# Optimization experiments

Measured on AMD Instinct MI355X. Metric: run time of the kernel, lower is better.

## Reference

```python
import jax, jax.numpy as jnp
import numpy as np

B, T, V, E, H = 32, 40, 8000, 50, 2048


def setup_inputs() -> dict:
    key = jax.random.key(0)
    ks = jax.random.split(key, 13)
    s = 0.02  # small init scale for stability
    return {
        "features": jax.random.normal(ks[0], (B, H), dtype=jnp.float32),
        "captions": jax.random.randint(ks[1], (B, T), 0, V),
        "emb": jax.random.normal(ks[2], (V, E), dtype=jnp.float32) * s,
        "lstm_Wih": jax.random.normal(ks[3], (4 * H, E), dtype=jnp.float32) * s,
        "lstm_bih": jax.random.normal(ks[4], (4 * H,), dtype=jnp.float32) * s,
        "lstm_Whh": jax.random.normal(ks[5], (4 * H, H), dtype=jnp.float32) * s,
        "lstm_bhh": jax.random.normal(ks[6], (4 * H,), dtype=jnp.float32) * s,
        "gru_Wih": jax.random.normal(ks[7], (3 * H, H), dtype=jnp.float32) * s,
        "gru_bih": jax.random.normal(ks[8], (3 * H,), dtype=jnp.float32) * s,
        "gru_Whh": jax.random.normal(ks[9], (3 * H, H), dtype=jnp.float32) * s,
        "gru_bhh": jax.random.normal(ks[10], (3 * H,), dtype=jnp.float32) * s,
        "lin_W": jax.random.normal(ks[11], (V, H), dtype=jnp.float32) * s,
        "lin_b": jax.random.normal(ks[12], (V,), dtype=jnp.float32) * s,
    }


def reference(features, captions, emb, lstm_Wih, lstm_bih, lstm_Whh, lstm_bhh,
              gru_Wih, gru_bih, gru_Whh, gru_bhh, lin_W, lin_b):
    # Dropout layers act as identity in eval mode.
    embeddings = emb[captions]                 # [B, T, E]
    xs = jnp.swapaxes(embeddings[:, :-1], 0, 1)  # [T-1, B, E]

    def step(carry, x):
        h_l, c_l, h_g = carry
        # torch LSTMCell
        gates = x @ lstm_Wih.T + lstm_bih + h_l @ lstm_Whh.T + lstm_bhh
        i, f, g, o = jnp.split(gates, 4, axis=-1)
        c = jax.nn.sigmoid(f) * c_l + jax.nn.sigmoid(i) * jnp.tanh(g)
        h = jax.nn.sigmoid(o) * jnp.tanh(c)
        # torch GRUCell, input = lstm cell state c
        gi = c @ gru_Wih.T + gru_bih
        gh = h_g @ gru_Whh.T + gru_bhh
        r_i, z_i, n_i = jnp.split(gi, 3, axis=-1)
        r_h, z_h, n_h = jnp.split(gh, 3, axis=-1)
        r = jax.nn.sigmoid(r_i + r_h)
        z = jax.nn.sigmoid(z_i + z_h)
        n = jnp.tanh(n_i + r * n_h)
        hg = (1.0 - z) * n + z * h_g
        out = hg @ lin_W.T + lin_b              # [B, V]
        return (h, c, hg), out

    init = (features, features, features)
    _, outs = jax.lax.scan(step, init, xs)      # [T-1, B, V]
    return jnp.swapaxes(outs, 0, 1)             # [B, T-1, V]
```

## Files before the change

### kernel.cpp

```cpp
#include <hip/hip_runtime.h>

#define BB 32
#define TT 40
#define TS 39
#define VV 8000
#define EE 50
#define HH 2048

typedef short s16x8 __attribute__((ext_vector_type(8)));
typedef float f32x4 __attribute__((ext_vector_type(4)));

__device__ __forceinline__ float sigmf(float x) { return 1.0f / (1.0f + __expf(-x)); }
__device__ __forceinline__ float tanhf_fast(float x) { return 2.0f / (1.0f + __expf(-2.0f * x)) - 1.0f; }

__device__ __forceinline__ unsigned short f2bf(float x) {
    union { float f; unsigned u; } v; v.f = x;
    unsigned r = v.u + 0x7FFF + ((v.u >> 16) & 1);
    return (unsigned short)(r >> 16);
}

__global__ void convert_kernel(const float* __restrict__ src,
                               unsigned short* __restrict__ dst, int n4) {
    int i = blockIdx.x * 256 + threadIdx.x;
    if (i < n4) {
        float4 v = ((const float4*)src)[i];
        ushort4 o;
        o.x = f2bf(v.x); o.y = f2bf(v.y); o.z = f2bf(v.z); o.w = f2bf(v.w);
        ((ushort4*)dst)[i] = o;
    }
}

__global__ void embed_proj_kernel(const int* __restrict__ caps,
                                  const float* __restrict__ emb,
                                  const float* __restrict__ Wih,
                                  const float* __restrict__ bih,
                                  const float* __restrict__ bhh,
                                  float* __restrict__ xw) {
    __shared__ float elds[BB][EE];
    int t = blockIdx.y;
    int j = blockIdx.x * 256 + threadIdx.x;
    for (int idx = threadIdx.x; idx < BB * EE; idx += 256) {
        int bl = idx / EE, e = idx - bl * EE;
        elds[bl][e] = emb[(size_t)caps[bl * TT + t] * EE + e];
    }
    __syncthreads();
    float wreg[EE];
#pragma unroll
    for (int e = 0; e < EE; ++e) wreg[e] = Wih[(size_t)j * EE + e];
    float bias = bih[j] + bhh[j];
    for (int bl = 0; bl < BB; ++bl) {
        float acc = bias;
#pragma unroll
        for (int e = 0; e < EE; ++e) acc += wreg[e] * elds[bl][e];
        xw[((size_t)(t * BB + bl)) * (4 * HH) + j] = acc;
    }
}

__global__ void init_state_kernel(const float* __restrict__ feat,
                                  float* __restrict__ c32, float* __restrict__ hg32,
                                  unsigned short* __restrict__ hbf,
                                  unsigned short* __restrict__ cbf,
                                  unsigned short* __restrict__ hgbf) {
    int i = blockIdx.x * 256 + threadIdx.x;
    float v = feat[i];
    c32[i] = v; hg32[i] = v;
    unsigned short b = f2bf(v);
    hbf[i] = b; cbf[i] = b; hgbf[i] = b;
}

__global__ __launch_bounds__(1024, 4) void step1_kernel(
    const unsigned short* __restrict__ Whh,
    const unsigned short* __restrict__ gWhh,
    const float* __restrict__ gbhh,
    const float* __restrict__ xw_t,
    const unsigned short* __restrict__ hbf_in,
    const unsigned short* __restrict__ hgbf,
    float* __restrict__ c32,
    unsigned short* __restrict__ cbf,
    unsigned short* __restrict__ hbf_out,
    float* __restrict__ gh)
{
    __shared__ float lsum[4][4][32][17];
    const int tid = threadIdx.x;
    const int lane = tid & 63;
    const int w = tid >> 6;
    const int g = w >> 2;
    const int kh = w & 3;
    const int l15 = lane & 15;
    const int lq = lane >> 4;
    const int kofs = kh * 512 + lq * 8;

    const bool lstm = (blockIdx.x < 128);
    const unsigned short* Abase;
    const unsigned short* Brow;
    if (lstm) {
        int kk0 = blockIdx.x * 16;
        Brow = Whh + (size_t)(g * HH + kk0 + l15) * HH + kofs;
        Abase = hbf_in;
    } else {
        int n0 = (blockIdx.x - 128) * 64;
        Brow = gWhh + (size_t)(n0 + g * 16 + l15) * HH + kofs;
        Abase = hgbf;
    }
    const unsigned short* Arow0 = Abase + l15 * HH + kofs;
    const unsigned short* Arow1 = Arow0 + 16 * HH;

    f32x4 acc0 = {0.f, 0.f, 0.f, 0.f};
    f32x4 acc1 = {0.f, 0.f, 0.f, 0.f};
#pragma unroll 4
    for (int it = 0; it < 16; ++it) {
        s16x8 bv = *(const s16x8*)(Brow + it * 32);
        s16x8 a0 = *(const s16x8*)(Arow0 + it * 32);
        s16x8 a1 = *(const s16x8*)(Arow1 + it * 32);
        acc0 = __builtin_amdgcn_mfma_f32_16x16x32_bf16(a0, bv, acc0, 0, 0, 0);
        acc1 = __builtin_amdgcn_mfma_f32_16x16x32_bf16(a1, bv, acc1, 0, 0, 0);
    }
#pragma unroll
    for (int r = 0; r < 4; ++r) {
        lsum[g][kh][lq * 4 + r][l15]      = acc0[r];
        lsum[g][kh][16 + lq * 4 + r][l15] = acc1[r];
    }
    __syncthreads();

    if (lstm) {
        if (tid < 512) {
            int kk0 = blockIdx.x * 16;
            int kkl = tid & 15, b = tid >> 4;
            int kk = kk0 + kkl;
            const float* xwb = xw_t + (size_t)b * 4 * HH;
            float vi = lsum[0][0][b][kkl] + lsum[0][1][b][kkl] + lsum[0][2][b][kkl] + lsum[0][3][b][kkl] + xwb[kk];
            float vf = lsum[1][0][b][kkl] + lsum[1][1][b][kkl] + lsum[1][2][b][kkl] + lsum[1][3][b][kkl] + xwb[HH + kk];
            float vg = lsum[2][0][b][kkl] + lsum[2][1][b][kkl] + lsum[2][2][b][kkl] + lsum[2][3][b][kkl] + xwb[2 * HH + kk];
            float vo = lsum[3][0][b][kkl] + lsum[3][1][b][kkl] + lsum[3][2][b][kkl] + lsum[3][3][b][kkl] + xwb[3 * HH + kk];
            int idx = b * HH + kk;
            float c = sigmf(vf) * c32[idx] + sigmf(vi) * tanhf_fast(vg);
            float h = sigmf(vo) * tanhf_fast(c);
            c32[idx] = c;
            cbf[idx] = f2bf(c);
            hbf_out[idx] = f2bf(h);
        }
    } else {
        int n0 = (blockIdx.x - 128) * 64;
        for (int cell = tid; cell < 2048; cell += 1024) {
            int nl = cell & 63, b = cell >> 6;
            int s = nl >> 4, n15 = nl & 15;
            float v = lsum[s][0][b][n15] + lsum[s][1][b][n15] + lsum[s][2][b][n15] + lsum[s][3][b][n15]
                      + gbhh[n0 + nl];
            gh[b * 3 * HH + n0 + nl] = v;
        }
    }
}

__global__ __launch_bounds__(768, 3) void step2_kernel(
    const unsigned short* __restrict__ gWih,
    const float* __restrict__ gbih,
    const unsigned short* __restrict__ cbf,
    const float* __restrict__ gh,
    float* __restrict__ hg32,
    unsigned short* __restrict__ hgbf,
    unsigned short* __restrict__ hg_all_t)
{
    __shared__ float lsum[3][4][32][17];
    const int tid = threadIdx.x;
    const int lane = tid & 63;
    const int w = tid >> 6;
    const int g = w >> 2;
    const int kh = w & 3;
    const int l15 = lane & 15;
    const int lq = lane >> 4;
    const int kofs = kh * 512 + lq * 8;
    const int kk0 = blockIdx.x * 16;

    const unsigned short* Arow0 = cbf + l15 * HH + kofs;
    const unsigned short* Arow1 = Arow0 + 16 * HH;
    const unsigned short* Brow = gWih + (size_t)(g * HH + kk0 + l15) * HH + kofs;

    f32x4 acc0 = {0.f, 0.f, 0.f, 0.f};
    f32x4 acc1 = {0.f, 0.f, 0.f, 0.f};
#pragma unroll 4
    for (int it = 0; it < 16; ++it) {
        s16x8 bv = *(const s16x8*)(Brow + it * 32);
        s16x8 a0 = *(const s16x8*)(Arow0 + it * 32);
        s16x8 a1 = *(const s16x8*)(Arow1 + it * 32);
        acc0 = __builtin_amdgcn_mfma_f32_16x16x32_bf16(a0, bv, acc0, 0, 0, 0);
        acc1 = __builtin_amdgcn_mfma_f32_16x16x32_bf16(a1, bv, acc1, 0, 0, 0);
    }
#pragma unroll
    for (int r = 0; r < 4; ++r) {
        lsum[g][kh][lq * 4 + r][l15]      = acc0[r];
        lsum[g][kh][16 + lq * 4 + r][l15] = acc1[r];
    }
    __syncthreads();

    if (tid < 512) {
        int kkl = tid & 15, b = tid >> 4;
        int kk = kk0 + kkl;
        float ri = lsum[0][0][b][kkl] + lsum[0][1][b][kkl] + lsum[0][2][b][kkl] + lsum[0][3][b][kkl] + gbih[kk];
        float zi = lsum[1][0][b][kkl] + lsum[1][1][b][kkl] + lsum[1][2][b][kkl] + lsum[1][3][b][kkl] + gbih[HH + kk];
        float ni = lsum[2][0][b][kkl] + lsum[2][1][b][kkl] + lsum[2][2][b][kkl] + lsum[2][3][b][kkl] + gbih[2 * HH + kk];
        const float* ghb = gh + b * 3 * HH;
        float r = sigmf(ri + ghb[kk]);
        float z = sigmf(zi + ghb[HH + kk]);
        float n = tanhf_fast(ni + r * ghb[2 * HH + kk]);
        int idx = b * HH + kk;
        float hgn = (1.f - z) * n + z * hg32[idx];
        hg32[idx] = hgn;
        unsigned short hb = f2bf(hgn);
        hgbf[idx] = hb;
        hg_all_t[idx] = hb;
    }
}

__global__ __launch_bounds__(256) void out_gemm_kernel(
    const unsigned short* __restrict__ A,
    const unsigned short* __restrict__ Wl,
    const float* __restrict__ bl,
    float* __restrict__ out) {
    __shared__ unsigned short As[128][32];
    __shared__ unsigned short Bs[128][32];
    const int tid = threadIdx.x;
    const int lane = tid & 63;
    const int w = tid >> 6;
    const int l15 = lane & 15;
    const int lq = lane >> 4;
    const int mt = blockIdx.x, nt = blockIdx.y;
    const int mq = w >> 1, nq = w & 1;

    const int row0 = tid >> 2, kc0 = (tid & 3) * 8;
    const unsigned short* Ap0 = A + (size_t)(mt * 128 + row0) * HH + kc0;
    const unsigned short* Ap1 = A + (size_t)(mt * 128 + 64 + row0) * HH + kc0;
    const unsigned short* Bp0 = Wl + (size_t)(nt * 128 + row0) * HH + kc0;
    const unsigned short* Bp1 = Wl + (size_t)(nt * 128 + 64 + row0) * HH + kc0;

    f32x4 acc[4][4];
#pragma unroll
    for (int i = 0; i < 4; ++i)
#pragma unroll
        for (int j = 0; j < 4; ++j) acc[i][j] = (f32x4){0.f, 0.f, 0.f, 0.f};

    for (int k0 = 0; k0 < HH; k0 += 32) {
        s16x8 a0v = *(const s16x8*)(Ap0 + k0);
        s16x8 a1v = *(const s16x8*)(Ap1 + k0);
        s16x8 b0v = *(const s16x8*)(Bp0 + k0);
        s16x8 b1v = *(const s16x8*)(Bp1 + k0);
        *(s16x8*)&As[row0][kc0]      = a0v;
        *(s16x8*)&As[64 + row0][kc0] = a1v;
        *(s16x8*)&Bs[row0][kc0]      = b0v;
        *(s16x8*)&Bs[64 + row0][kc0] = b1v;
        __syncthreads();
        s16x8 af[4], bf[4];
#pragma unroll
        for (int i = 0; i < 4; ++i) af[i] = *(const s16x8*)&As[mq * 64 + i * 16 + l15][lq * 8];
#pragma unroll
        for (int j = 0; j < 4; ++j) bf[j] = *(const s16x8*)&Bs[nq * 64 + j * 16 + l15][lq * 8];
#pragma unroll
        for (int i = 0; i < 4; ++i)
#pragma unroll
            for (int j = 0; j < 4; ++j)
                acc[i][j] = __builtin_amdgcn_mfma_f32_16x16x32_bf16(af[i], bf[j], acc[i][j], 0, 0, 0);
        __syncthreads();
    }
#pragma unroll
    for (int j = 0; j < 4; ++j) {
        int n = nt * 128 + nq * 64 + j * 16 + l15;
        float bn = bl[n < VV ? n : VV - 1];
#pragma unroll
        for (int i = 0; i < 4; ++i) {
#pragma unroll
            for (int r = 0; r < 4; ++r) {
                int m = mt * 128 + mq * 64 + i * 16 + lq * 4 + r;
                if (m < TS * BB && n < VV) {
                    int t = m >> 5, b = m & 31;
                    out[((size_t)b * TS + t) * VV + n] = acc[i][j][r] + bn;
                }
            }
        }
    }
}

extern "C" void kernel_launch(void* const* d_in, const int* in_sizes, int n_in,
                              void* d_out, int out_size, void* d_ws, size_t ws_size,
                              hipStream_t stream) {
    const float* features = (const float*)d_in[0];
    const int*   captions = (const int*)d_in[1];
    const float* emb      = (const float*)d_in[2];
    const float* lstm_Wih = (const float*)d_in[3];
    const float* lstm_bih = (const float*)d_in[4];
    const float* lstm_Whh = (const float*)d_in[5];
    const float* lstm_bhh = (const float*)d_in[6];
    const float* gru_Wih  = (const float*)d_in[7];
    const float* gru_bih  = (const float*)d_in[8];
    const float* gru_Whh  = (const float*)d_in[9];
    const float* gru_bhh  = (const float*)d_in[10];
    const float* lin_W    = (const float*)d_in[11];
    const float* lin_b    = (const float*)d_in[12];
    float* out = (float*)d_out;

    unsigned short* us = (unsigned short*)d_ws;
    unsigned short* Whh_bf  = us;
    unsigned short* gWhh_bf = Whh_bf  + (size_t)8192 * HH;
    unsigned short* gWih_bf = gWhh_bf + (size_t)6144 * HH;
    unsigned short* linW_bf = gWih_bf + (size_t)6144 * HH;
    unsigned short* hbf0    = linW_bf + (size_t)VV * HH;
    unsigned short* hbf1    = hbf0 + BB * HH;
    unsigned short* cbf     = hbf1 + BB * HH;
    unsigned short* hgbf    = cbf  + BB * HH;
    unsigned short* hg_all  = hgbf + BB * HH;
    float* f32s = (float*)(hg_all + (size_t)1280 * HH);
    float* xw   = f32s;
    float* c32  = xw + (size_t)TS * BB * 4 * HH;
    float* hg32 = c32 + BB * HH;
    float* gh   = hg32 + BB * HH;

    {
        int n4;
        n4 = 8192 * HH / 4;
        convert_kernel<<<(n4 + 255) / 256, 256, 0, stream>>>(lstm_Whh, Whh_bf, n4);
        n4 = 6144 * HH / 4;
        convert_kernel<<<(n4 + 255) / 256, 256, 0, stream>>>(gru_Whh, gWhh_bf, n4);
        convert_kernel<<<(n4 + 255) / 256, 256, 0, stream>>>(gru_Wih, gWih_bf, n4);
        n4 = VV * HH / 4;
        convert_kernel<<<(n4 + 255) / 256, 256, 0, stream>>>(lin_W, linW_bf, n4);
    }

    embed_proj_kernel<<<dim3(4 * HH / 256, TS), 256, 0, stream>>>(
        captions, emb, lstm_Wih, lstm_bih, lstm_bhh, xw);

    init_state_kernel<<<(BB * HH) / 256, 256, 0, stream>>>(
        features, c32, hg32, hbf0, cbf, hgbf);

    for (int t = 0; t < TS; ++t) {
        const unsigned short* hin = (t & 1) ? hbf1 : hbf0;
        unsigned short*       hout = (t & 1) ? hbf0 : hbf1;
        step1_kernel<<<224, 1024, 0, stream>>>(
            Whh_bf, gWhh_bf, gru_bhh, xw + (size_t)t * BB * 4 * HH,
            hin, hgbf, c32, cbf, hout, gh);
        step2_kernel<<<128, 768, 0, stream>>>(
            gWih_bf, gru_bih, cbf, gh, hg32, hgbf, hg_all + (size_t)t * BB * HH);
    }

    out_gemm_kernel<<<dim3((TS * BB + 127) / 128, (VV + 127) / 128), 256, 0, stream>>>(
        hg_all, linW_bf, lin_b, out);
}
```

Baseline: 2.053 ms.

## Fuse per-timestep recurrence kernels into one persistent kernel with grid barriers

Replaces the 78 per-step launches of step1/step2 with one persistent recurrence kernel of 224 blocks that loops over all timesteps. An atomic-counter grid barrier separates the LSTM/GRU-hidden phase from the GRU-input phase. This removes kernel launch overhead and inter-kernel gaps. In exchange, all blocks must be co-resident or the barrier deadlocks, and the spin barrier adds its own latency. Non-LSTM blocks sit idle during the second phase.

Result: slower. 3.850 ms (+87.6%).

```diff
diff --git a/kernel.cpp b/kernel.cpp
--- a/kernel.cpp
+++ b/kernel.cpp
@@ -6,6 +6,7 @@
 #define VV 8000
 #define EE 50
 #define HH 2048
+#define NBLK 224
 
 typedef short s16x8 __attribute__((ext_vector_type(8)));
 typedef float f32x4 __attribute__((ext_vector_type(4)));
@@ -60,25 +61,42 @@
                                   float* __restrict__ c32, float* __restrict__ hg32,
                                   unsigned short* __restrict__ hbf,
                                   unsigned short* __restrict__ cbf,
-                                  unsigned short* __restrict__ hgbf) {
+                                  unsigned short* __restrict__ hgbf,
+                                  unsigned int* __restrict__ bar) {
     int i = blockIdx.x * 256 + threadIdx.x;
     float v = feat[i];
     c32[i] = v; hg32[i] = v;
     unsigned short b = f2bf(v);
     hbf[i] = b; cbf[i] = b; hgbf[i] = b;
-}
-
-__global__ __launch_bounds__(1024, 4) void step1_kernel(
+    if (i == 0) *bar = 0u;
+}
+
+__device__ __forceinline__ void grid_sync(unsigned int* bar, unsigned int target) {
+    __syncthreads();
+    if (threadIdx.x == 0) {
+        __hip_atomic_fetch_add(bar, 1u, __ATOMIC_RELEASE, __HIP_MEMORY_SCOPE_AGENT);
+        while (__hip_atomic_load(bar, __ATOMIC_ACQUIRE, __HIP_MEMORY_SCOPE_AGENT) < target)
+            __builtin_amdgcn_s_sleep(2);
+    }
+    __syncthreads();
+}
+
+__global__ __launch_bounds__(1024, 4) void recurrence_kernel(
     const unsigned short* __restrict__ Whh,
     const unsigned short* __restrict__ gWhh,
+    const unsigned short* __restrict__ gWih,
     const float* __restrict__ gbhh,
-    const float* __restrict__ xw_t,
-    const unsigned short* __restrict__ hbf_in,
-    const unsigned short* __restrict__ hgbf,
+    const float* __restrict__ gbih,
+    const float* __restrict__ xw,
+    unsigned short* __restrict__ hbf0,
+    unsigned short* __restrict__ hbf1,
+    unsigned short* __restrict__ hgbf,
+    unsigned short* __restrict__ cbf,
     float* __restrict__ c32,
-    unsigned short* __restrict__ cbf,
-    unsigned short* __restrict__ hbf_out,
-    float* __restrict__ gh)
+    float* __restrict__ hg32,
+    float* __restrict__ gh,
+    unsigned short* __restrict__ hg_all,
+    unsigned int* bar)
 {
     __shared__ float lsum[4][4][32][17];
     const int tid = threadIdx.x;
@@ -89,125 +107,116 @@
     const int l15 = lane & 15;
     const int lq = lane >> 4;
     const int kofs = kh * 512 + lq * 8;
-
-    const bool lstm = (blockIdx.x < 128);
-    const unsigned short* Abase;
-    const unsigned short* Brow;
-    if (lstm) {
-        int kk0 = blockIdx.x * 16;
-        Brow = Whh + (size_t)(g * HH + kk0 + l15) * HH + kofs;
-        Abase = hbf_in;
-    } else {
-        int n0 = (blockIdx.x - 128) * 64;
-        Brow = gWhh + (size_t)(n0 + g * 16 + l15) * HH + kofs;
-        Abase = hgbf;
-    }
-    const unsigned short* Arow0 = Abase + l15 * HH + kofs;
-    const unsigned short* Arow1 = Arow0 + 16 * HH;
-
-    f32x4 acc0 = {0.f, 0.f, 0.f, 0.f};
-    f32x4 acc1 = {0.f, 0.f, 0.f, 0.f};
+    const int bx = blockIdx.x;
+    const bool lstm = (bx < 128);
+
+    const unsigned short* Brow1 = lstm
+        ? Whh  + (size_t)(g * HH + bx * 16 + l15) * HH + kofs
+        : gWhh + (size_t)((bx - 128) * 64 + g * 16 + l15) * HH + kofs;
+
+    const int g2  = (w < 12) ? g : 0;
+    const int bx2 = lstm ? bx : 0;
+    const unsigned short* Brow2  = gWih + (size_t)(g2 * HH + bx2 * 16 + l15) * HH + kofs;
+    const unsigned short* A2row0 = cbf + l15 * HH + kofs;
+    const unsigned short* A2row1 = A2row0 + 16 * HH;
+
+    unsigned int nbar = 0;
+
+    for (int t = 0; t < TS; ++t) {
+        const unsigned short* hin  = (t & 1) ? hbf1 : hbf0;
+        unsigned short*       hout = (t & 1) ? hbf0 : hbf1;
+        const float* xw_t = xw + (size_t)t * BB * 4 * HH;
+
+        {
+            const unsigned short* Abase = lstm ? hin : hgbf;
+            const unsigned short* Arow0 = Abase + l15 * HH + kofs;
+            const unsigned short* Arow1 = Arow0 + 16 * HH;
+            f32x4 acc0 = {0.f, 0.f, 0.f, 0.f};
+            f32x4 acc1 = {0.f, 0.f, 0.f, 0.f};
 #pragma unroll 4
-    for (int it = 0; it < 16; ++it) {
-        s16x8 bv = *(const s16x8*)(Brow + it * 32);
-        s16x8 a0 = *(const s16x8*)(Arow0 + it * 32);
-        s16x8 a1 = *(const s16x8*)(Arow1 + it * 32);
-        acc0 = __builtin_amdgcn_mfma_f32_16x16x32_bf16(a0, bv, acc0, 0, 0, 0);
-        acc1 = __builtin_amdgcn_mfma_f32_16x16x32_bf16(a1, bv, acc1, 0, 0, 0);
-    }
-#pragma unroll
-    for (int r = 0; r < 4; ++r) {
-        lsum[g][kh][lq * 4 + r][l15]      = acc0[r];
-        lsum[g][kh][16 + lq * 4 + r][l15] = acc1[r];
-    }
-    __syncthreads();
-
-    if (lstm) {
-        if (tid < 512) {
-            int kk0 = blockIdx.x * 16;
-            int kkl = tid & 15, b = tid >> 4;
-            int kk = kk0 + kkl;
-            const float* xwb = xw_t + (size_t)b * 4 * HH;
-            float vi = lsum[0][0][b][kkl] + lsum[0][1][b][kkl] + lsum[0][2][b][kkl] + lsum[0][3][b][kkl] + xwb[kk];
-            float vf = lsum[1][0][b][kkl] + lsum[1][1][b][kkl] + lsum[1][2][b][kkl] + lsum[1][3][b][kkl] + xwb[HH + kk];
-            float vg = lsum[2][0][b][kkl] + lsum[2][1][b][kkl] + lsum[2][2][b][kkl] + lsum[2][3][b][kkl] + xwb[2 * HH + kk];
-            float vo = lsum[3][0][b][kkl] + lsum[3][1][b][kkl] + lsum[3][2][b][kkl] + lsum[3][3][b][kkl] + xwb[3 * HH + kk];
-            int idx = b * HH + kk;
-            float c = sigmf(vf) * c32[idx] + sigmf(vi) * tanhf_fast(vg);
-            float h = sigmf(vo) * tanhf_fast(c);
-            c32[idx] = c;
-            cbf[idx] = f2bf(c);
-            hbf_out[idx] = f2bf(h);
+            for (int it = 0; it < 16; ++it) {
+                s16x8 bv = *(const s16x8*)(Brow1 + it * 32);
+                s16x8 a0 = *(const s16x8*)(Arow0 + it * 32);
+                s16x8 a1 = *(const s16x8*)(Arow1 + it * 32);
+                acc0 = __builtin_amdgcn_mfma_f32_16x16x32_bf16(a0, bv, acc0, 0, 0, 0);
+                acc1 = __builtin_amdgcn_mfma_f32_16x16x32_bf16(a1, bv, acc1, 0, 0, 0);
+            }
+#pragma unroll
+            for (int r = 0; r < 4; ++r) {
+                lsum[g][kh][lq * 4 + r][l15]      = acc0[r];
+                lsum[g][kh][16 + lq * 4 + r][l15] = acc1[r];
+            }
+            __syncthreads();
+
+            if (lstm) {
+                if (tid < 512) {
+                    int kk0 = bx * 16;
+                    int kkl = tid & 15, b = tid >> 4;
+                    int kk = kk0 + kkl;
+                    const float* xwb = xw_t + (size_t)b * 4 * HH;
+                    float vi = lsum[0][0][b][kkl] + lsum[0][1][b][kkl] + lsum[0][2][b][kkl] + lsum[0][3][b][kkl] + xwb[kk];
+                    float vf = lsum[1][0][b][kkl] + lsum[1][1][b][kkl] + lsum[1][2][b][kkl] + lsum[1][3][b][kkl] + xwb[HH + kk];
+                    float vg = lsum[2][0][b][kkl] + lsum[2][1][b][kkl] + lsum[2][2][b][kkl] + lsum[2][3][b][kkl] + xwb[2 * HH + kk];
+                    float vo = lsum[3][0][b][kkl] + lsum[3][1][b][kkl] + lsum[3][2][b][kkl] + lsum[3][3][b][kkl] + xwb[3 * HH + kk];
+                    int idx = b * HH + kk;
+                    float c = sigmf(vf) * c32[idx] + sigmf(vi) * tanhf_fast(vg);
+                    float h = sigmf(vo) * tanhf_fast(c);
+                    c32[idx] = c;
+                    cbf[idx] = f2bf(c);
+                    hout[idx] = f2bf(h);
+                }
+            } else {
+                int n0 = (bx - 128) * 64;
+                for (int cell = tid; cell < 2048; cell += 1024) {
+                    int nl = cell & 63, b = cell >> 6;
+                    int s = nl >> 4, n15 = nl & 15;
+                    float v = lsum[s][0][b][n15] + lsum[s][1][b][n15] + lsum[s][2][b][n15] + lsum[s][3][b][n15]
+                              + gbhh[n0 + nl];
+                    gh[b * 3 * HH + n0 + nl] = v;
+                }
+            }
         }
-    } else {
-        int n0 = (blockIdx.x - 128) * 64;
-        for (int cell = tid; cell < 2048; cell += 1024) {
-            int nl = cell & 63, b = cell >> 6;
-            int s = nl >> 4, n15 = nl & 15;
-            float v = lsum[s][0][b][n15] + lsum[s][1][b][n15] + lsum[s][2][b][n15] + lsum[s][3][b][n15]
-                      + gbhh[n0 + nl];
-            gh[b * 3 * HH + n0 + nl] = v;
+        grid_sync(bar, ++nbar * NBLK);
+
+        if (lstm) {
+            if (w < 12) {
+                f32x4 acc0 = {0.f, 0.f, 0.f, 0.f};
+                f32x4 acc1 = {0.f, 0.f, 0.f, 0.f};
+#pragma unroll 4
+                for (int it = 0; it < 16; ++it) {
+                    s16x8 bv = *(const s16x8*)(Brow2 + it * 32);
+                    s16x8 a0 = *(const s16x8*)(A2row0 + it * 32);
+                    s16x8 a1 = *(const s16x8*)(A2row1 + it * 32);
+                    acc0 = __builtin_amdgcn_mfma_f32_16x16x32_bf16(a0, bv, acc0, 0, 0, 0);
+                    acc1 = __builtin_amdgcn_mfma_f32_16x16x32_bf16(a1, bv, acc1, 0, 0, 0);
+                }
+#pragma unroll
+                for (int r = 0; r < 4; ++r) {
+                    lsum[g][kh][lq * 4 + r][l15]      = acc0[r];
+                    lsum[g][kh][16 + lq * 4 + r][l15] = acc1[r];
+                }
+            }
+            __syncthreads();
+
+            if (tid < 512) {
+                int kkl = tid & 15, b = tid >> 4;
+                int kk = bx * 16 + kkl;
+                float ri = lsum[0][0][b][kkl] + lsum[0][1][b][kkl] + lsum[0][2][b][kkl] + lsum[0][3][b][kkl] + gbih[kk];
+                float zi = lsum[1][0][b][kkl] + lsum[1][1][b][kkl] + lsum[1][2][b][kkl] + lsum[1][3][b][kkl] + gbih[HH + kk];
+                float ni = lsum[2][0][b][kkl] + lsum[2][1][b][kkl] + lsum[2][2][b][kkl] + lsum[2][3][b][kkl] + gbih[2 * HH + kk];
+                const float* ghb = gh + b * 3 * HH;
+                float r = sigmf(ri + ghb[kk]);
+                float z = sigmf(zi + ghb[HH + kk]);
+                float n = tanhf_fast(ni + r * ghb[2 * HH + kk]);
+                int idx = b * HH + kk;
+                float hgn = (1.f - z) * n + z * hg32[idx];
+                hg32[idx] = hgn;
+                unsigned short hb = f2bf(hgn);
+                hgbf[idx] = hb;
+                hg_all[(size_t)t * BB * HH + idx] = hb;
+            }
         }
-    }
-}
-
-__global__ __launch_bounds__(768, 3) void step2_kernel(
-    const unsigned short* __restrict__ gWih,
-    const float* __restrict__ gbih,
-    const unsigned short* __restrict__ cbf,
-    const float* __restrict__ gh,
-    float* __restrict__ hg32,
-    unsigned short* __restrict__ hgbf,
-    unsigned short* __restrict__ hg_all_t)
-{
-    __shared__ float lsum[3][4][32][17];
-    const int tid = threadIdx.x;
-    const int lane = tid & 63;
-    const int w = tid >> 6;
-    const int g = w >> 2;
-    const int kh = w & 3;
-    const int l15 = lane & 15;
-    const int lq = lane >> 4;
-    const int kofs = kh * 512 + lq * 8;
-    const int kk0 = blockIdx.x * 16;
-
-    const unsigned short* Arow0 = cbf + l15 * HH + kofs;
-    const unsigned short* Arow1 = Arow0 + 16 * HH;
-    const unsigned short* Brow = gWih + (size_t)(g * HH + kk0 + l15) * HH + kofs;
-
-    f32x4 acc0 = {0.f, 0.f, 0.f, 0.f};
-    f32x4 acc1 = {0.f, 0.f, 0.f, 0.f};
-#pragma unroll 4
-    for (int it = 0; it < 16; ++it) {
-        s16x8 bv = *(const s16x8*)(Brow + it * 32);
-        s16x8 a0 = *(const s16x8*)(Arow0 + it * 32);
-        s16x8 a1 = *(const s16x8*)(Arow1 + it * 32);
-        acc0 = __builtin_amdgcn_mfma_f32_16x16x32_bf16(a0, bv, acc0, 0, 0, 0);
-        acc1 = __builtin_amdgcn_mfma_f32_16x16x32_bf16(a1, bv, acc1, 0, 0, 0);
-    }
-#pragma unroll
-    for (int r = 0; r < 4; ++r) {
-        lsum[g][kh][lq * 4 + r][l15]      = acc0[r];
-        lsum[g][kh][16 + lq * 4 + r][l15] = acc1[r];
-    }
-    __syncthreads();
-
-    if (tid < 512) {
-        int kkl = tid & 15, b = tid >> 4;
-        int kk = kk0 + kkl;
-        float ri = lsum[0][0][b][kkl] + lsum[0][1][b][kkl] + lsum[0][2][b][kkl] + lsum[0][3][b][kkl] + gbih[kk];
-        float zi = lsum[1][0][b][kkl] + lsum[1][1][b][kkl] + lsum[1][2][b][kkl] + lsum[1][3][b][kkl] + gbih[HH + kk];
-        float ni = lsum[2][0][b][kkl] + lsum[2][1][b][kkl] + lsum[2][2][b][kkl] + lsum[2][3][b][kkl] + gbih[2 * HH + kk];
-        const float* ghb = gh + b * 3 * HH;
-        float r = sigmf(ri + ghb[kk]);
-        float z = sigmf(zi + ghb[HH + kk]);
-        float n = tanhf_fast(ni + r * ghb[2 * HH + kk]);
-        int idx = b * HH + kk;
-        float hgn = (1.f - z) * n + z * hg32[idx];
-        hg32[idx] = hgn;
-        unsigned short hb = f2bf(hgn);
-        hgbf[idx] = hb;
-        hg_all_t[idx] = hb;
+        grid_sync(bar, ++nbar * NBLK);
     }
 }
 
@@ -311,6 +320,7 @@
     float* c32  = xw + (size_t)TS * BB * 4 * HH;
     float* hg32 = c32 + BB * HH;
     float* gh   = hg32 + BB * HH;
+    unsigned int* bar = (unsigned int*)(gh + (size_t)BB * 3 * HH);
 
     {
         int n4;
@@ -327,17 +337,11 @@
         captions, emb, lstm_Wih, lstm_bih, lstm_bhh, xw);
 
     init_state_kernel<<<(BB * HH) / 256, 256, 0, stream>>>(
-        features, c32, hg32, hbf0, cbf, hgbf);
-
-    for (int t = 0; t < TS; ++t) {
-        const unsigned short* hin = (t & 1) ? hbf1 : hbf0;
-        unsigned short*       hout = (t & 1) ? hbf0 : hbf1;
-        step1_kernel<<<224, 1024, 0, stream>>>(
-            Whh_bf, gWhh_bf, gru_bhh, xw + (size_t)t * BB * 4 * HH,
-            hin, hgbf, c32, cbf, hout, gh);
-        step2_kernel<<<128, 768, 0, stream>>>(
-            gWih_bf, gru_bih, cbf, gh, hg32, hgbf, hg_all + (size_t)t * BB * HH);
-    }
+        features, c32, hg32, hbf0, cbf, hgbf, bar);
+
+    recurrence_kernel<<<NBLK, 1024, 0, stream>>>(
+        Whh_bf, gWhh_bf, gWih_bf, gru_bhh, gru_bih, xw,
+        hbf0, hbf1, hgbf, cbf, c32, hg32, gh, hg_all, bar);
 
     out_gemm_kernel<<<dim3((TS * BB + 127) / 128, (VV + 127) / 128), 256, 0, stream>>>(
         hg_all, linW_bf, lin_b, out);
```
